# Kernel optimization log

Hardware: AMD Instinct MI355X
Metric: run time of the kernel (lower is better)

The kernel has to match this reference:

```python
import jax, jax.numpy as jnp
import numpy as np

PD = 256            # pretrain_dim == dim_in (standard mode)
DZ = 128            # dim_z
PD2 = PD + 2        # feature dim after concatenating 2-d coords
FD = PD + 2 * PD2   # final_dim = 772
TEMP = float(DZ) ** 0.5
EPS = 1e-12
N1, N2 = 4096, 2048


def _lin_init(key, din, dout):
    w = jax.random.normal(key, (dout, din), jnp.float32) * 0.02
    b = jnp.zeros((dout,), jnp.float32)
    return w, b


def _lin(x, w, b):
    return x @ w.T + b


def setup_inputs() -> dict:
    key = jax.random.key(0)
    ks = jax.random.split(key, 13)
    lm_X = jax.random.normal(ks[0], (N1, PD), jnp.float32)
    lm_Y = jax.random.normal(ks[1], (N1, 2), jnp.float32)
    tg_X = jax.random.normal(ks[2], (N2, PD), jnp.float32)
    tg_Y = jax.random.normal(ks[3], (N2, 2), jnp.float32)
    lm_delay = jax.random.uniform(ks[4], (N1,), jnp.float32)
    tg_delay = jax.random.uniform(ks[5], (N2,), jnp.float32)
    aq_w, aq_b = _lin_init(ks[6], PD, DZ)    # att_attribute q proj
    ak_w, ak_b = _lin_init(ks[7], PD, DZ)    # att_attribute k proj
    w1_w, w1_b = _lin_init(ks[8], PD2, PD2)  # self.w_1
    w2_w, w2_b = _lin_init(ks[9], PD2, PD2)  # self.w_2
    pq_w, pq_b = _lin_init(ks[10], FD, DZ)   # pred attention q proj
    pk_w, pk_b = _lin_init(ks[11], PD, DZ)   # pred attention k proj
    pv_w, pv_b = _lin_init(ks[12], 2, 2)     # pred attention v proj
    gamma1 = jnp.ones((1, 1), jnp.float32)
    gamma2 = jnp.ones((1, 1), jnp.float32)
    gamma3 = jnp.ones((1, 1), jnp.float32)
    alpha = jnp.ones((1, 1), jnp.float32)
    beta = jnp.zeros((1, 1), jnp.float32)
    return dict(lm_X=lm_X, lm_Y=lm_Y, tg_X=tg_X, tg_Y=tg_Y,
                lm_delay=lm_delay, tg_delay=tg_delay,
                aq_w=aq_w, aq_b=aq_b, ak_w=ak_w, ak_b=ak_b,
                w1_w=w1_w, w1_b=w1_b, w2_w=w2_w, w2_b=w2_b,
                pq_w=pq_w, pq_b=pq_b, pk_w=pk_w, pk_b=pk_b,
                pv_w=pv_w, pv_b=pv_b,
                gamma1=gamma1, gamma2=gamma2, gamma3=gamma3,
                alpha=alpha, beta=beta)


def reference(lm_X, lm_Y, tg_X, tg_Y, lm_delay, tg_delay,
              aq_w, aq_b, ak_w, ak_b,
              w1_w, w1_b, w2_w, w2_b,
              pq_w, pq_b, pk_w, pk_b, pv_w, pv_b,
              gamma1, gamma2, gamma3, alpha, beta):
    n2 = tg_X.shape[0]
    a = alpha[0, 0]
    b0 = beta[0, 0]

    lm_feature = jnp.concatenate([lm_X, lm_Y], axis=1)            # [N1, PD2]
    tg_feature_0 = jnp.concatenate([tg_X, jnp.zeros((n2, 2), lm_X.dtype)], axis=1)
    router_0 = jnp.mean(lm_feature, axis=0)                        # [PD2]

    delay_score = jnp.exp(-gamma1[0, 0] * (a * lm_delay + b0))     # [N1]
    rou0 = jnp.exp(-gamma2[0, 0] * (a * tg_delay + b0))            # [N2]
    rou1 = jnp.exp(-gamma3[0, 0] * (a * tg_delay + b0))            # [N2]

    # SimpleAttention1: attribute score of targets over landmarks
    q = _lin(tg_X, aq_w, aq_b)
    k = _lin(lm_X, ak_w, ak_b)
    attr = jnp.exp(jax.nn.softmax((q / TEMP) @ k.T, axis=-1))      # [N2, N1]

    # Degree-normalized propagation of adj_matrix_0 (block-structured:
    # lm rows = identity, tg rows = [attr | I | rou0-col], router row = [delay | 0 | 1]).
    deg_tg0 = 1.0 + attr.sum(axis=1) + rou0                        # [N2]
    tg_prop0 = (attr @ lm_feature + tg_feature_0 + rou0[:, None] * router_0[None, :]) \
               / (deg_tg0 + EPS)[:, None]
    router_prop0 = (delay_score @ lm_feature + router_0) / (1.0 + delay_score.sum() + EPS)

    tg_feature_1 = _lin(tg_prop0, w1_w, w1_b)                      # [N2, PD2]
    router_1 = _lin(router_prop0[None, :], w1_w, w1_b)             # [1, PD2]

    # Second propagation: adj_matrix_1 = I + rou1 on tg->router column.
    tg_prop1 = (tg_feature_1 + rou1[:, None] * router_1) / (1.0 + rou1 + EPS)[:, None]
    tg_feature_2 = _lin(tg_prop1, w2_w, w2_b)                      # [N2, PD2]

    final_tg_feature = jnp.concatenate([tg_X, tg_feature_1, tg_feature_2], axis=-1)  # [N2, FD]

    # SimpleAttention2 (collaborative MLP prediction)
    q2 = _lin(final_tg_feature, pq_w, pq_b)
    k2 = _lin(lm_X, pk_w, pk_b)
    v2 = _lin(lm_Y, pv_w, pv_b)
    attn2 = jax.nn.softmax((q2 / TEMP) @ k2.T, axis=-1)            # [N2, N1]
    y_pred = attn2 @ v2                                            # [N2, 2]
    return y_pred, final_tg_feature
```

## Files before the change

kernel.cpp:

```cpp
#include <hip/hip_runtime.h>

#define N1 4096
#define N2 2048
#define PD 256
#define DZ 128
#define PD2 258
#define PD2P 264
#define FD 772
#define FDP 776
#define APN 272
#define APLD 72
#define SPLITS 16

typedef short s8v __attribute__((ext_vector_type(8)));
typedef float f32x4 __attribute__((ext_vector_type(4)));

__device__ __forceinline__ short f2b(float f) {
    union { float f; unsigned u; } v; v.f = f;
    unsigned r = v.u + 0x7fffu + ((v.u >> 16) & 1u);
    return (short)(r >> 16);
}
__device__ __forceinline__ float sb2f(short s) {
    union { unsigned u; float f; } v;
    v.u = ((unsigned)(unsigned short)s) << 16;
    return v.f;
}

constexpr int R0 = N2 * PD;
constexpr int R1 = R0 + PD2 * PD2P;
constexpr int R2 = R1 + PD2 * PD2P;
constexpr int R3 = R2 + DZ * FDP;
constexpr int R4 = R3 + APN * N1;
constexpr int R5 = R4 + 4096;
constexpr int R6 = R5 + 2048;
constexpr int R7 = R6 + N2 * 4;
constexpr int R8 = R7 + N2 * 6;

__global__ __launch_bounds__(256) void cvt_all(
    const float* __restrict__ lmX, const float* __restrict__ lmY,
    const float* __restrict__ tgX,
    const float* __restrict__ pqw, const float* __restrict__ w1w,
    const float* __restrict__ w2w,
    const float* __restrict__ lmd, const float* __restrict__ tgd,
    const float* __restrict__ g1, const float* __restrict__ g2,
    const float* __restrict__ g3, const float* __restrict__ al,
    const float* __restrict__ be,
    const float* __restrict__ pvw, const float* __restrict__ pvb,
    short* __restrict__ w1wb, short* __restrict__ w2wb,
    short* __restrict__ pqwb, short* __restrict__ lmFTb,
    float* __restrict__ dscore, float* __restrict__ rou0,
    float* __restrict__ rou1, float* __restrict__ v2b,
    float* __restrict__ Z, short* __restrict__ finalFb,
    short* __restrict__ tgp1b, float* __restrict__ outF)
{
    int i = blockIdx.x * 256 + threadIdx.x;
    if (i < R0) { int r = i >> 8, c = i & 255;
                  float v = tgX[i];
                  outF[(size_t)r * FD + c] = v;
                  finalFb[(size_t)r * FDP + c] = f2b(v); return; }
    if (i < R1) { int j = i - R0; int r = j / PD2P, c = j - r * PD2P;
                  w1wb[j] = (c < PD2) ? f2b(w1w[r * PD2 + c]) : (short)0; return; }
    if (i < R2) { int j = i - R1; int r = j / PD2P, c = j - r * PD2P;
                  w2wb[j] = (c < PD2) ? f2b(w2w[r * PD2 + c]) : (short)0; return; }
    if (i < R3) { int j = i - R2; int r = j / FDP, c = j - r * FDP;
                  pqwb[j] = (c < FD) ? f2b(pqw[r * FD + c]) : (short)0; return; }
    if (i < R4) { int j = i - R3; int c = j >> 12, r = j & (N1 - 1);
                  float v = 0.f;
                  if (c < PD) v = lmX[(size_t)r * PD + c];
                  else if (c < PD2) v = lmY[r * 2 + (c - PD)];
                  else if (c == PD2) v = 1.0f;
                  lmFTb[j] = f2b(v); return; }
    if (i < R5) { int j = i - R4;
                  float a = al[0], b = be[0];
                  dscore[j] = __expf(-g1[0] * (a * lmd[j] + b));
                  float y0 = lmY[2 * j], y1 = lmY[2 * j + 1];
                  v2b[2 * j]     = pvw[0] * y0 + pvw[1] * y1 + pvb[0];
                  v2b[2 * j + 1] = pvw[2] * y0 + pvw[3] * y1 + pvb[1];
                  if (j < N2) { float t = a * tgd[j] + b;
                                rou0[j] = __expf(-g2[0] * t);
                                rou1[j] = __expf(-g3[0] * t); }
                  return; }
    if (i < R6) { Z[i - R5] = 0.f; return; }
    if (i < R7) { int j = i - R6; int r = j >> 2;
                  finalFb[(size_t)r * FDP + FD + (j & 3)] = 0; return; }
    if (i < R8) { int j = i - R7; int r = j / 6;
                  tgp1b[(size_t)r * PD2P + PD2 + (j - r * 6)] = 0; return; }
}

__global__ __launch_bounds__(256) void rkq_kernel(
    const float* __restrict__ lmX, const float* __restrict__ tgX,
    const float* __restrict__ aqw, const float* __restrict__ aqb,
    const float* __restrict__ akw, const float* __restrict__ akb,
    const float* __restrict__ pkw, const float* __restrict__ pkb,
    const short* __restrict__ lmFTb, const float* __restrict__ dscore,
    float* __restrict__ router0, float* __restrict__ routerp0,
    short* __restrict__ kk, short* __restrict__ qb)
{
    __shared__ __align__(16) short LDS[5120];
    const int j = blockIdx.x, tid = threadIdx.x;
    const int lane = tid & 63, wv = tid >> 6;
    const int wm = wv >> 1, wn = wv & 1;
    const int lm = lane & 15, lq = lane >> 4;
    const f32x4 zero4 = {0.f, 0.f, 0.f, 0.f};

    if (j < 258) {
        float* r1 = (float*)LDS;
        float* r2 = r1 + 256;
        float* r3 = r2 + 256;
        const short* rowp = lmFTb + (size_t)j * N1;
        float s1 = 0.f, s2 = 0.f, s3 = 0.f;
        for (int i = tid; i < N1; i += 256) {
            float v = sb2f(rowp[i]);
            float d = dscore[i];
            s1 += v; s2 += d * v; s3 += d;
        }
        r1[tid] = s1; r2[tid] = s2; r3[tid] = s3; __syncthreads();
        for (int o = 128; o > 0; o >>= 1) {
            if (tid < o) { r1[tid] += r1[tid + o]; r2[tid] += r2[tid + o]; r3[tid] += r3[tid + o]; }
            __syncthreads();
        }
        if (tid == 0) {
            float r0v = r1[0] / (float)N1;
            router0[j] = r0v;
            routerp0[j] = (r2[0] + r0v) / (1.f + r3[0] + 1e-12f);
        }
        return;
    }
    short* Als = LDS;
    short* Bls = LDS + 64 * 40;
    f32x4 acc[2][2] = {{zero4, zero4}, {zero4, zero4}};
    const int r = tid >> 2, cgp = tid & 3;
    if (j < 514) {
        int jt = j - 258;
        int row0 = (jt >> 2) * 64, col0 = (jt & 3) * 64;
        for (int k0 = 0; k0 < 256; k0 += 32) {
            int gk = k0 + cgp * 8;
            const float* ap = lmX + (size_t)(row0 + r) * PD + gk;
            int c = col0 + r;
            const float* bp = (c < 128) ? akw + (size_t)c * PD + gk
                                        : pkw + (size_t)(c - 128) * PD + gk;
            s8v va, vb;
#pragma unroll
            for (int q = 0; q < 8; ++q) { va[q] = f2b(ap[q]); vb[q] = f2b(bp[q]); }
            *(s8v*)(Als + r * 40 + cgp * 8) = va;
            *(s8v*)(Bls + r * 40 + cgp * 8) = vb;
            __syncthreads();
            s8v af[2], bf[2];
#pragma unroll
            for (int mt = 0; mt < 2; ++mt)
                af[mt] = *(const s8v*)(Als + (wm * 32 + mt * 16 + lm) * 40 + lq * 8);
#pragma unroll
            for (int nt = 0; nt < 2; ++nt)
                bf[nt] = *(const s8v*)(Bls + (wn * 32 + nt * 16 + lm) * 40 + lq * 8);
#pragma unroll
            for (int mt = 0; mt < 2; ++mt)
#pragma unroll
                for (int nt = 0; nt < 2; ++nt)
                    acc[mt][nt] = __builtin_amdgcn_mfma_f32_16x16x32_bf16(
                        af[mt], bf[nt], acc[mt][nt], 0, 0, 0);
            __syncthreads();
        }
#pragma unroll
        for (int mt = 0; mt < 2; ++mt)
#pragma unroll
            for (int nt = 0; nt < 2; ++nt) {
                int c = col0 + wn * 32 + nt * 16 + lm;
                float bv = (c < 128) ? akb[c] : pkb[c - 128];
#pragma unroll
                for (int i = 0; i < 4; ++i) {
                    int rr = row0 + wm * 32 + mt * 16 + lq * 4 + i;
                    kk[(size_t)rr * 256 + c] = f2b(acc[mt][nt][i] + bv);
                }
            }
    } else {
        int jt = j - 514;
        int row0 = (jt >> 1) * 64, col0 = (jt & 1) * 64;
        for (int k0 = 0; k0 < 256; k0 += 32) {
            int gk = k0 + cgp * 8;
            const float* ap = tgX + (size_t)(row0 + r) * PD + gk;
            const float* bp = aqw + (size_t)(col0 + r) * PD + gk;
            s8v va, vb;
#pragma unroll
            for (int q = 0; q < 8; ++q) { va[q] = f2b(ap[q]); vb[q] = f2b(bp[q]); }
            *(s8v*)(Als + r * 40 + cgp * 8) = va;
            *(s8v*)(Bls + r * 40 + cgp * 8) = vb;
            __syncthreads();
            s8v af[2], bf[2];
#pragma unroll
            for (int mt = 0; mt < 2; ++mt)
                af[mt] = *(const s8v*)(Als + (wm * 32 + mt * 16 + lm) * 40 + lq * 8);
#pragma unroll
            for (int nt = 0; nt < 2; ++nt)
                bf[nt] = *(const s8v*)(Bls + (wn * 32 + nt * 16 + lm) * 40 + lq * 8);
#pragma unroll
            for (int mt = 0; mt < 2; ++mt)
#pragma unroll
                for (int nt = 0; nt < 2; ++nt)
                    acc[mt][nt] = __builtin_amdgcn_mfma_f32_16x16x32_bf16(
                        af[mt], bf[nt], acc[mt][nt], 0, 0, 0);
            __syncthreads();
        }
        const float INV_TEMP = 0.08838834764831845f;
#pragma unroll
        for (int mt = 0; mt < 2; ++mt)
#pragma unroll
            for (int nt = 0; nt < 2; ++nt) {
                int c = col0 + wn * 32 + nt * 16 + lm;
                float bv = aqb[c];
#pragma unroll
                for (int i = 0; i < 4; ++i) {
                    int rr = row0 + wm * 32 + mt * 16 + lq * 4 + i;
                    qb[(size_t)rr * DZ + c] = f2b(INV_TEMP * (acc[mt][nt][i] + bv));
                }
            }
    }
}

__global__ __launch_bounds__(256) void scores_e(
    const short* __restrict__ Q, const short* __restrict__ Kk,
    short* __restrict__ E, float* __restrict__ Z,
    const float* __restrict__ rp0, const float* __restrict__ w1w,
    const float* __restrict__ w1b, float* __restrict__ router1)
{
    const int j = blockIdx.x, tid = threadIdx.x;
    if (j == 512) {
        for (int c = tid; c < PD2; c += 256) {
            float s = w1b[c];
            const float* wr = w1w + (size_t)c * PD2;
            for (int k = 0; k < PD2; ++k) s += rp0[k] * wr[k];
            router1[c] = s;
        }
        return;
    }
    __shared__ __align__(16) short LDS[10240];
    short* Als = LDS;
    short* Bls = LDS + 128 * 40;
    const int lane = tid & 63, wv = tid >> 6;
    const int wm = wv >> 1, wn = wv & 1;
    const int lm = lane & 15, lq = lane >> 4;
    const int row0 = (j >> 5) * 128, col0 = (j & 31) * 128;
    const f32x4 zero4 = {0.f, 0.f, 0.f, 0.f};
    f32x4 acc[4][4];
#pragma unroll
    for (int mt = 0; mt < 4; ++mt)
#pragma unroll
        for (int nt = 0; nt < 4; ++nt) acc[mt][nt] = zero4;
    for (int k0 = 0; k0 < 128; k0 += 32) {
#pragma unroll
        for (int l = 0; l < 2; ++l) {
            int id = l * 256 + tid;
            int r = id >> 2, cgp = id & 3;
            int gk = k0 + cgp * 8;
            *(s8v*)(Als + r * 40 + cgp * 8) = *(const s8v*)(Q + (size_t)(row0 + r) * DZ + gk);
            *(s8v*)(Bls + r * 40 + cgp * 8) = *(const s8v*)(Kk + (size_t)(col0 + r) * 256 + gk);
        }
        __syncthreads();
        s8v af[4], bf[4];
#pragma unroll
        for (int mt = 0; mt < 4; ++mt)
            af[mt] = *(const s8v*)(Als + (wm * 64 + mt * 16 + lm) * 40 + lq * 8);
#pragma unroll
        for (int nt = 0; nt < 4; ++nt)
            bf[nt] = *(const s8v*)(Bls + (wn * 64 + nt * 16 + lm) * 40 + lq * 8);
#pragma unroll
        for (int mt = 0; mt < 4; ++mt)
#pragma unroll
            for (int nt = 0; nt < 4; ++nt)
                acc[mt][nt] = __builtin_amdgcn_mfma_f32_16x16x32_bf16(
                    af[mt], bf[nt], acc[mt][nt], 0, 0, 0);
        __syncthreads();
    }
#pragma unroll
    for (int mt = 0; mt < 4; ++mt)
#pragma unroll
        for (int i = 0; i < 4; ++i) {
            int r = row0 + wm * 64 + mt * 16 + lq * 4 + i;
            float rs = 0.f;
#pragma unroll
            for (int nt = 0; nt < 4; ++nt) {
                int c = col0 + wn * 64 + nt * 16 + lm;
                float e = __expf(acc[mt][nt][i]);
                E[(size_t)r * N1 + c] = f2b(e);
                rs += e;
            }
#pragma unroll
            for (int msk = 1; msk < 16; msk <<= 1) rs += __shfl_xor(rs, msk, 64);
            if (lm == 0) atomicAdd(&Z[r], rs);
        }
}

__global__ __launch_bounds__(512) void ap_gemm(const short* __restrict__ E,
                                               const float* __restrict__ Z,
                                               const short* __restrict__ lmFTb,
                                               short* __restrict__ part)
{
    __shared__ __align__(16) short LDS[28800];
    const int tid = threadIdx.x, bid = blockIdx.x;
    const int lane = tid & 63, w8 = tid >> 6;
    const int lm = lane & 15, lq = lane >> 4;
    const int s = bid & 15, row0 = (bid >> 4) * 128;
    const int kbase = s * (N1 / SPLITS);
    short* Als = LDS;
    short* Bls = LDS + 128 * APLD;
    const f32x4 zero4 = {0.f, 0.f, 0.f, 0.f};
    f32x4 acc[17];
#pragma unroll
    for (int nt = 0; nt < 17; ++nt) acc[nt] = zero4;
    for (int it = 0; it < (N1 / SPLITS) / 64; ++it) {
        int k0 = kbase + it * 64;
#pragma unroll
        for (int l = 0; l < 2; ++l) {
            int id = l * 512 + tid;
            int r = id >> 3, gg = id & 7;
            s8v ev = *(const s8v*)(E + (size_t)(row0 + r) * N1 + k0 + gg * 8);
            float invZ = __builtin_amdgcn_rcpf(Z[row0 + r]);
            s8v av;
#pragma unroll
            for (int q = 0; q < 8; ++q)
                av[q] = f2b(__expf(sb2f(ev[q]) * invZ));
            *(s8v*)(Als + r * APLD + gg * 8) = av;
        }
#pragma unroll
        for (int l = 0; l < 5; ++l) {
            int id = l * 512 + tid;
            if (id < APN * 8) {
                int r = id >> 3, gg = id & 7;
                *(s8v*)(Bls + r * APLD + gg * 8) =
                    *(const s8v*)(lmFTb + (size_t)r * N1 + k0 + gg * 8);
            }
        }
        __syncthreads();
        s8v a0 = *(const s8v*)(Als + (w8 * 16 + lm) * APLD + lq * 8);
        s8v a1 = *(const s8v*)(Als + (w8 * 16 + lm) * APLD + 32 + lq * 8);
#pragma unroll
        for (int nt = 0; nt < 17; ++nt) {
            s8v b0 = *(const s8v*)(Bls + (nt * 16 + lm) * APLD + lq * 8);
            s8v b1 = *(const s8v*)(Bls + (nt * 16 + lm) * APLD + 32 + lq * 8);
            acc[nt] = __builtin_amdgcn_mfma_f32_16x16x32_bf16(a0, b0, acc[nt], 0, 0, 0);
            acc[nt] = __builtin_amdgcn_mfma_f32_16x16x32_bf16(a1, b1, acc[nt], 0, 0, 0);
        }
        __syncthreads();
    }
    short* op = part + (size_t)s * N2 * APN;
#pragma unroll
    for (int nt = 0; nt < 17; ++nt) {
        int c = nt * 16 + lm;
#pragma unroll
        for (int i = 0; i < 4; ++i) {
            int r = row0 + w8 * 16 + lq * 4 + i;
            op[(size_t)r * APN + c] = f2b(acc[nt][i]);
        }
    }
}

__global__ __launch_bounds__(256) void fix_tgp0(const short* __restrict__ part,
                                                const float* __restrict__ tgX,
                                                const float* __restrict__ rou0,
                                                const float* __restrict__ router0,
                                                short* __restrict__ outb) {
    int r = blockIdx.x;
    int tid = threadIdx.x;
    __shared__ float sAsum;
    float s0 = 0.f, s1 = 0.f;
#pragma unroll
    for (int s = 0; s < SPLITS; ++s)
        s0 += sb2f(part[((size_t)s * N2 + r) * APN + tid]);
    if (tid < 8) {
#pragma unroll
        for (int s = 0; s < SPLITS; ++s)
            s1 += sb2f(part[((size_t)s * N2 + r) * APN + 256 + tid]);
    }
    if (tid == 2) sAsum = s1;
    __syncthreads();
    float ro = rou0[r];
    float inv = 1.f / (1.f + sAsum + ro + 1e-12f);
    {
        float v = (s0 + tgX[(size_t)r * PD + tid] + ro * router0[tid]) * inv;
        outb[(size_t)r * PD2P + tid] = f2b(v);
    }
    if (tid < 8) {
        int c = 256 + tid;
        float v = 0.f;
        if (c < PD2) v = (s1 + ro * router0[c]) * inv;
        outb[(size_t)r * PD2P + c] = f2b(v);
    }
}

__global__ __launch_bounds__(256) void w_gemm(
    const short* __restrict__ A, const short* __restrict__ B,
    const float* __restrict__ bias,
    float* __restrict__ outFcol, short* __restrict__ fFbcol,
    const float* __restrict__ rou1, const float* __restrict__ router1,
    short* __restrict__ tgp1b)
{
    __shared__ __align__(16) short LDS[5120];
    short* Als = LDS;
    short* Bls = LDS + 64 * 40;
    const int tid = threadIdx.x;
    const int lane = tid & 63, wv = tid >> 6;
    const int wm = wv >> 1, wn = wv & 1;
    const int lm = lane & 15, lq = lane >> 4;
    const int row0 = blockIdx.y * 64, col0 = blockIdx.x * 64;
    const f32x4 zero4 = {0.f, 0.f, 0.f, 0.f};
    f32x4 acc[2][2] = {{zero4, zero4}, {zero4, zero4}};
    const s8v zero8 = {0, 0, 0, 0, 0, 0, 0, 0};
    const int r = tid >> 2, cgp = tid & 3;
    for (int k0 = 0; k0 < PD2P; k0 += 32) {
        int gk = k0 + cgp * 8;
        s8v va = zero8, vb = zero8;
        if (gk < PD2P) {
            va = *(const s8v*)(A + (size_t)(row0 + r) * PD2P + gk);
            if (col0 + r < PD2) vb = *(const s8v*)(B + (size_t)(col0 + r) * PD2P + gk);
        }
        *(s8v*)(Als + r * 40 + cgp * 8) = va;
        *(s8v*)(Bls + r * 40 + cgp * 8) = vb;
        __syncthreads();
        s8v af[2], bf[2];
#pragma unroll
        for (int mt = 0; mt < 2; ++mt)
            af[mt] = *(const s8v*)(Als + (wm * 32 + mt * 16 + lm) * 40 + lq * 8);
#pragma unroll
        for (int nt = 0; nt < 2; ++nt)
            bf[nt] = *(const s8v*)(Bls + (wn * 32 + nt * 16 + lm) * 40 + lq * 8);
#pragma unroll
        for (int mt = 0; mt < 2; ++mt)
#pragma unroll
            for (int nt = 0; nt < 2; ++nt)
                acc[mt][nt] = __builtin_amdgcn_mfma_f32_16x16x32_bf16(
                    af[mt], bf[nt], acc[mt][nt], 0, 0, 0);
        __syncthreads();
    }
#pragma unroll
    for (int mt = 0; mt < 2; ++mt)
#pragma unroll
        for (int nt = 0; nt < 2; ++nt) {
            int c = col0 + wn * 32 + nt * 16 + lm;
            if (c >= PD2) continue;
            float bv = bias[c];
            float rc = router1 ? router1[c] : 0.f;
#pragma unroll
            for (int i = 0; i < 4; ++i) {
                int rr = row0 + wm * 32 + mt * 16 + lq * 4 + i;
                float v = acc[mt][nt][i] + bv;
                outFcol[(size_t)rr * FD + c] = v;
                fFbcol[(size_t)rr * FDP + c] = f2b(v);
                if (tgp1b) {
                    float ro = rou1[rr];
                    tgp1b[(size_t)rr * PD2P + c] =
                        f2b((v + ro * rc) / (1.f + ro + 1e-12f));
                }
            }
        }
}

__global__ __launch_bounds__(256) void q2_gemm(
    const short* __restrict__ A, const short* __restrict__ B,
    const float* __restrict__ bias, short* __restrict__ outB)
{
    __shared__ __align__(16) short LDS[5120];
    short* Als = LDS;
    short* Bls = LDS + 64 * 40;
    const int tid = threadIdx.x;
    const int lane = tid & 63, wv = tid >> 6;
    const int wm = wv >> 1, wn = wv & 1;
    const int lm = lane & 15, lq = lane >> 4;
    const int row0 = blockIdx.y * 64, col0 = blockIdx.x * 64;
    const f32x4 zero4 = {0.f, 0.f, 0.f, 0.f};
    f32x4 acc[2][2] = {{zero4, zero4}, {zero4, zero4}};
    const s8v zero8 = {0, 0, 0, 0, 0, 0, 0, 0};
    const int r = tid >> 2, cgp = tid & 3;
    for (int k0 = 0; k0 < FDP; k0 += 32) {
        int gk = k0 + cgp * 8;
        s8v va = zero8, vb = zero8;
        if (gk < FDP) {
            va = *(const s8v*)(A + (size_t)(row0 + r) * FDP + gk);
            vb = *(const s8v*)(B + (size_t)(col0 + r) * FDP + gk);
        }
        *(s8v*)(Als + r * 40 + cgp * 8) = va;
        *(s8v*)(Bls + r * 40 + cgp * 8) = vb;
        __syncthreads();
        s8v af[2], bf[2];
#pragma unroll
        for (int mt = 0; mt < 2; ++mt)
            af[mt] = *(const s8v*)(Als + (wm * 32 + mt * 16 + lm) * 40 + lq * 8);
#pragma unroll
        for (int nt = 0; nt < 2; ++nt)
            bf[nt] = *(const s8v*)(Bls + (wn * 32 + nt * 16 + lm) * 40 + lq * 8);
#pragma unroll
        for (int mt = 0; mt < 2; ++mt)
#pragma unroll
            for (int nt = 0; nt < 2; ++nt)
                acc[mt][nt] = __builtin_amdgcn_mfma_f32_16x16x32_bf16(
                    af[mt], bf[nt], acc[mt][nt], 0, 0, 0);
        __syncthreads();
    }
    const float INV_TEMP = 0.08838834764831845f;
#pragma unroll
    for (int mt = 0; mt < 2; ++mt)
#pragma unroll
        for (int nt = 0; nt < 2; ++nt) {
            int c = col0 + wn * 32 + nt * 16 + lm;
            float bv = bias[c];
#pragma unroll
            for (int i = 0; i < 4; ++i) {
                int rr = row0 + wm * 32 + mt * 16 + lq * 4 + i;
                outB[(size_t)rr * DZ + c] = f2b(INV_TEMP * (acc[mt][nt][i] + bv));
            }
        }
}

__global__ __launch_bounds__(256) void attn2_flash(
    const short* __restrict__ Q, const short* __restrict__ Kk,
    const float* __restrict__ V, float* __restrict__ part2)
{
    __shared__ __align__(16) short Qls[64 * 136];
    __shared__ __align__(16) short Kls[64 * 136];
    __shared__ float Vls[128];
    const int tid = threadIdx.x;
    const int lane = tid & 63, wv = tid >> 6;
    const int lm = lane & 15, lq = lane >> 4;
    const int chunk = blockIdx.x & 15, row0 = (blockIdx.x >> 4) * 64;
    const f32x4 zero4 = {0.f, 0.f, 0.f, 0.f};
#pragma unroll
    for (int l = 0; l < 4; ++l) {
        int id = l * 256 + tid;
        int r = id >> 4, g = id & 15;
        *(s8v*)(Qls + r * 136 + g * 8) = *(const s8v*)(Q + (size_t)(row0 + r) * DZ + g * 8);
    }
    __syncthreads();
    s8v af[4];
#pragma unroll
    for (int ks = 0; ks < 4; ++ks)
        af[ks] = *(const s8v*)(Qls + (wv * 16 + lm) * 136 + ks * 32 + lq * 8);
    float z[4] = {0.f, 0.f, 0.f, 0.f};
    float y0[4] = {0.f, 0.f, 0.f, 0.f};
    float y1[4] = {0.f, 0.f, 0.f, 0.f};
    for (int t = 0; t < 4; ++t) {
        int col0 = chunk * 256 + t * 64;
        __syncthreads();
#pragma unroll
        for (int l = 0; l < 4; ++l) {
            int id = l * 256 + tid;
            int r = id >> 4, g = id & 15;
            *(s8v*)(Kls + r * 136 + g * 8) =
                *(const s8v*)(Kk + (size_t)(col0 + r) * 256 + 128 + g * 8);
        }
        if (tid < 128) Vls[tid] = V[col0 * 2 + tid];
        __syncthreads();
        f32x4 acc[4];
#pragma unroll
        for (int nt = 0; nt < 4; ++nt) acc[nt] = zero4;
#pragma unroll
        for (int nt = 0; nt < 4; ++nt)
#pragma unroll
            for (int ks = 0; ks < 4; ++ks) {
                s8v bf = *(const s8v*)(Kls + (nt * 16 + lm) * 136 + ks * 32 + lq * 8);
                acc[nt] = __builtin_amdgcn_mfma_f32_16x16x32_bf16(af[ks], bf, acc[nt], 0, 0, 0);
            }
        float v0[4], v1[4];
#pragma unroll
        for (int nt = 0; nt < 4; ++nt) {
            v0[nt] = Vls[(nt * 16 + lm) * 2];
            v1[nt] = Vls[(nt * 16 + lm) * 2 + 1];
        }
#pragma unroll
        for (int i = 0; i < 4; ++i) {
            float e0 = __expf(acc[0][i]), e1 = __expf(acc[1][i]);
            float e2 = __expf(acc[2][i]), e3 = __expf(acc[3][i]);
            z[i]  += e0 + e1 + e2 + e3;
            y0[i] += e0 * v0[0] + e1 * v0[1] + e2 * v0[2] + e3 * v0[3];
            y1[i] += e0 * v1[0] + e1 * v1[1] + e2 * v1[2] + e3 * v1[3];
        }
    }
#pragma unroll
    for (int i = 0; i < 4; ++i) {
#pragma unroll
        for (int msk = 1; msk < 16; msk <<= 1) {
            z[i]  += __shfl_xor(z[i], msk, 64);
            y0[i] += __shfl_xor(y0[i], msk, 64);
            y1[i] += __shfl_xor(y1[i], msk, 64);
        }
    }
    if (lm == 0) {
#pragma unroll
        for (int i = 0; i < 4; ++i) {
            int r = row0 + wv * 16 + lq * 4 + i;
            float* pp = part2 + ((size_t)r * 16 + chunk) * 4;
            pp[0] = z[i]; pp[1] = y0[i]; pp[2] = y1[i];
        }
    }
}

__global__ void attn2_combine(const float* __restrict__ part2, float* __restrict__ out) {
    int r = blockIdx.x * 256 + threadIdx.x;
    if (r >= N2) return;
    const float* pp = part2 + (size_t)r * 64;
    float Zt = 0.f, Y0 = 0.f, Y1 = 0.f;
#pragma unroll
    for (int c = 0; c < 16; ++c) {
        Zt += pp[c * 4]; Y0 += pp[c * 4 + 1]; Y1 += pp[c * 4 + 2];
    }
    out[2 * r] = Y0 / Zt;
    out[2 * r + 1] = Y1 / Zt;
}

extern "C" void kernel_launch(void* const* d_in, const int* in_sizes, int n_in,
                              void* d_out, int out_size, void* d_ws, size_t ws_size,
                              hipStream_t stream) {
    const float* lm_X = (const float*)d_in[0];
    const float* lm_Y = (const float*)d_in[1];
    const float* tg_X = (const float*)d_in[2];
    const float* lm_delay = (const float*)d_in[4];
    const float* tg_delay = (const float*)d_in[5];
    const float* aq_w = (const float*)d_in[6];
    const float* aq_b = (const float*)d_in[7];
    const float* ak_w = (const float*)d_in[8];
    const float* ak_b = (const float*)d_in[9];
    const float* w1_w = (const float*)d_in[10];
    const float* w1_b = (const float*)d_in[11];
    const float* w2_w = (const float*)d_in[12];
    const float* w2_b = (const float*)d_in[13];
    const float* pq_w = (const float*)d_in[14];
    const float* pq_b = (const float*)d_in[15];
    const float* pk_w = (const float*)d_in[16];
    const float* pk_b = (const float*)d_in[17];
    const float* pv_w = (const float*)d_in[18];
    const float* pv_b = (const float*)d_in[19];
    const float* g1 = (const float*)d_in[20];
    const float* g2 = (const float*)d_in[21];
    const float* g3 = (const float*)d_in[22];
    const float* al = (const float*)d_in[23];
    const float* be = (const float*)d_in[24];

    float* out = (float*)d_out;
    float* outF = out + (size_t)N2 * 2;

    char* base = (char*)d_ws;
    size_t off = 0;
    auto allocF = [&](size_t n) -> float* {
        float* q = (float*)(base + off);
        off += (n * 4 + 255) / 256 * 256;
        return q;
    };
    auto allocS = [&](size_t n) -> short* {
        short* q = (short*)(base + off);
        off += (n * 2 + 255) / 256 * 256;
        return q;
    };

    short* E        = allocS((size_t)N2 * N1);
    short* appart   = allocS((size_t)SPLITS * N2 * APN);
    short* lmFTb    = allocS((size_t)APN * N1);
    short* qb       = allocS((size_t)N2 * DZ);
    short* kk       = allocS((size_t)N1 * 256);
    short* q2       = allocS((size_t)N2 * DZ);
    short* tgp0b    = allocS((size_t)N2 * PD2P);
    short* tgp1b    = allocS((size_t)N2 * PD2P);
    short* finalFb  = allocS((size_t)N2 * FDP);
    short* w1wb     = allocS((size_t)PD2 * PD2P);
    short* w2wb     = allocS((size_t)PD2 * PD2P);
    short* pqwb     = allocS((size_t)DZ * FDP);
    float* v2b      = allocF((size_t)N1 * 2);
    float* part2    = allocF((size_t)N2 * 64);
    float* Zbuf     = allocF(N2);
    float* router0  = allocF(PD2);
    float* routerp0 = allocF(PD2);
    float* router1  = allocF(PD2);
    float* dscore   = allocF(N1);
    float* rou0     = allocF(N2);
    float* rou1     = allocF(N2);

    hipLaunchKernelGGL(cvt_all, dim3((R8 + 255) / 256), dim3(256), 0, stream,
                       lm_X, lm_Y, tg_X, pq_w, w1_w, w2_w,
                       lm_delay, tg_delay, g1, g2, g3, al, be, pv_w, pv_b,
                       w1wb, w2wb, pqwb, lmFTb,
                       dscore, rou0, rou1, v2b, Zbuf, finalFb, tgp1b, outF);
    hipLaunchKernelGGL(rkq_kernel, dim3(578), dim3(256), 0, stream,
                       lm_X, tg_X, aq_w, aq_b, ak_w, ak_b, pk_w, pk_b,
                       lmFTb, dscore, router0, routerp0, kk, qb);
    hipLaunchKernelGGL(scores_e, dim3(513), dim3(256), 0, stream,
                       qb, kk, E, Zbuf, routerp0, w1_w, w1_b, router1);
    hipLaunchKernelGGL(ap_gemm, dim3(256), dim3(512), 0, stream, E, Zbuf, lmFTb, appart);
    hipLaunchKernelGGL(fix_tgp0, dim3(N2), dim3(256), 0, stream,
                       appart, tg_X, rou0, router0, tgp0b);
    hipLaunchKernelGGL(w_gemm, dim3(5, 32), dim3(256), 0, stream,
                       tgp0b, w1wb, w1_b, outF + 256, finalFb + 256, rou1, router1, tgp1b);
    hipLaunchKernelGGL(w_gemm, dim3(5, 32), dim3(256), 0, stream,
                       tgp1b, w2wb, w2_b, outF + 514, finalFb + 514,
                       nullptr, nullptr, nullptr);
    hipLaunchKernelGGL(q2_gemm, dim3(2, 32), dim3(256), 0, stream,
                       finalFb, pqwb, pq_b, q2);
    hipLaunchKernelGGL(attn2_flash, dim3(512), dim3(256), 0, stream,
                       q2, kk, v2b, part2);
    hipLaunchKernelGGL(attn2_combine, dim3(8), dim3(256), 0, stream, part2, out);
}
```

Measured before the change: 219.4 us.

## Fold w1/w2 chain into combined weight, pre-convert inputs, fuse combine via atomics

Precomputes the combined weight W2·W1 so tg_feature_1 and tg_feature_2 come from tgp0 in a single merged GEMM launch, with the router and bias terms folded in algebraically. Converts lm_X, tg_X and the projection weights to bf16 once, and computes the router column sums inside the conversion kernel through an LDS transpose. The separate attn2 combine kernel is replaced by atomic accumulation and a last-block-done counter. This removes two launches and a serial GEMM dependency, at the cost of extra precompute, bf16 rounding of the combined weight, and atomic contention.

```diff
diff --git a/kernel.cpp b/kernel.cpp
--- a/kernel.cpp
+++ b/kernel.cpp
@@ -26,53 +26,126 @@
     return v.f;
 }
 
-constexpr int R0 = N2 * PD;
-constexpr int R1 = R0 + PD2 * PD2P;
-constexpr int R2 = R1 + PD2 * PD2P;
-constexpr int R3 = R2 + DZ * FDP;
-constexpr int R4 = R3 + APN * N1;
-constexpr int R5 = R4 + 4096;
-constexpr int R6 = R5 + 2048;
-constexpr int R7 = R6 + N2 * 4;
-constexpr int R8 = R7 + N2 * 6;
+constexpr int Q0 = N2 * PD;
+constexpr int Q1 = Q0 + PD2 * PD2P;
+constexpr int Q2 = Q1 + PD2 * PD2P;
+constexpr int Q3 = Q2 + PD2 * PD2P;
+constexpr int Q4 = Q3 + DZ * FDP;
+constexpr int Q5 = Q4 + 3 * DZ * PD;
+constexpr int Q6 = Q5 + 16 * N1;
+constexpr int Q7 = Q6 + N1;
+constexpr int Q8 = Q7 + N2;
+constexpr int Q9 = Q8 + N2 * 4;
+constexpr int Q10 = Q9 + N2 * 4;
+constexpr int Q11 = Q10 + 256;
+constexpr int TB = 256;
+constexpr int CVT_GRID = TB + (Q11 + 255) / 256;
 
 __global__ __launch_bounds__(256) void cvt_all(
     const float* __restrict__ lmX, const float* __restrict__ lmY,
     const float* __restrict__ tgX,
-    const float* __restrict__ pqw, const float* __restrict__ w1w,
-    const float* __restrict__ w2w,
+    const float* __restrict__ aqw, const float* __restrict__ akw,
+    const float* __restrict__ pkw, const float* __restrict__ pqw,
+    const float* __restrict__ w1w, const float* __restrict__ w2w,
     const float* __restrict__ lmd, const float* __restrict__ tgd,
     const float* __restrict__ g1, const float* __restrict__ g2,
     const float* __restrict__ g3, const float* __restrict__ al,
     const float* __restrict__ be,
     const float* __restrict__ pvw, const float* __restrict__ pvb,
     short* __restrict__ w1wb, short* __restrict__ w2wb,
-    short* __restrict__ pqwb, short* __restrict__ lmFTb,
-    float* __restrict__ dscore, float* __restrict__ rou0,
-    float* __restrict__ rou1, float* __restrict__ v2b,
-    float* __restrict__ Z, short* __restrict__ finalFb,
-    short* __restrict__ tgp1b, float* __restrict__ outF)
+    short* __restrict__ w1wtb, short* __restrict__ pqwb,
+    short* __restrict__ aqwb, short* __restrict__ akwb,
+    short* __restrict__ pkwb, short* __restrict__ lmXb,
+    short* __restrict__ tgXb, short* __restrict__ lmFTb,
+    float* __restrict__ rou0, float* __restrict__ rou1,
+    float* __restrict__ v2b, float* __restrict__ Z,
+    short* __restrict__ finalFb, float* __restrict__ outF,
+    float* __restrict__ r1part, float* __restrict__ r2part,
+    float* __restrict__ p2acc, unsigned* __restrict__ cnt)
 {
-    int i = blockIdx.x * 256 + threadIdx.x;
-    if (i < R0) { int r = i >> 8, c = i & 255;
-                  float v = tgX[i];
+    __shared__ __align__(16) short T[64][72];
+    __shared__ float dsc[64];
+    __shared__ float sp1[4][64];
+    __shared__ float sp2[4][64];
+    const int tid = threadIdx.x;
+
+    if (blockIdx.x < TB) {
+        const int rb = blockIdx.x >> 2, cb = blockIdx.x & 3;
+        const int r0 = rb * 64, c0 = cb * 64;
+        const int rr = tid >> 2, cg = tid & 3;
+        const float* src = lmX + (size_t)(r0 + rr) * PD + c0 + cg * 16;
+        f32x4 f0 = *(const f32x4*)(src);
+        f32x4 f1 = *(const f32x4*)(src + 4);
+        f32x4 f2v = *(const f32x4*)(src + 8);
+        f32x4 f3v = *(const f32x4*)(src + 12);
+        s8v h0, h1;
+#pragma unroll
+        for (int q = 0; q < 4; ++q) {
+            h0[q] = f2b(f0[q]); h0[4 + q] = f2b(f1[q]);
+            h1[q] = f2b(f2v[q]); h1[4 + q] = f2b(f3v[q]);
+        }
+        short* xb = lmXb + (size_t)(r0 + rr) * PD + c0 + cg * 16;
+        *(s8v*)(xb) = h0; *(s8v*)(xb + 8) = h1;
+        *(s8v*)(&T[rr][cg * 16]) = h0;
+        *(s8v*)(&T[rr][cg * 16 + 8]) = h1;
+        if (cg == 0) dsc[rr] = __expf(-g1[0] * (al[0] * lmd[r0 + rr] + be[0]));
+        __syncthreads();
+        {
+            const int c = tid & 63, q = tid >> 6;
+            float s1 = 0.f, s2 = 0.f;
+#pragma unroll
+            for (int k = 0; k < 16; ++k) {
+                float x = sb2f(T[q * 16 + k][c]);
+                s1 += x; s2 += dsc[q * 16 + k] * x;
+            }
+            sp1[q][c] = s1; sp2[q][c] = s2;
+        }
+        __syncthreads();
+        if (tid < 64) {
+            float S1 = sp1[0][tid] + sp1[1][tid] + sp1[2][tid] + sp1[3][tid];
+            float S2 = sp2[0][tid] + sp2[1][tid] + sp2[2][tid] + sp2[3][tid];
+            r1part[(size_t)(c0 + tid) * 64 + rb] = S1;
+            r2part[(size_t)(c0 + tid) * 64 + rb] = S2;
+        }
+        {
+            const int c = tid >> 2, seg = tid & 3;
+            s8v o0, o1;
+#pragma unroll
+            for (int k = 0; k < 8; ++k) {
+                o0[k] = T[seg * 16 + k][c];
+                o1[k] = T[seg * 16 + 8 + k][c];
+            }
+            short* dst = lmFTb + (size_t)(c0 + c) * N1 + r0 + seg * 16;
+            *(s8v*)(dst) = o0; *(s8v*)(dst + 8) = o1;
+        }
+        return;
+    }
+
+    int i = (blockIdx.x - TB) * 256 + tid;
+    if (i < Q0) { int r = i >> 8, c = i & 255;
+                  float v = tgX[i]; short h = f2b(v);
                   outF[(size_t)r * FD + c] = v;
-                  finalFb[(size_t)r * FDP + c] = f2b(v); return; }
-    if (i < R1) { int j = i - R0; int r = j / PD2P, c = j - r * PD2P;
+                  finalFb[(size_t)r * FDP + c] = h;
+                  tgXb[i] = h; return; }
+    if (i < Q1) { int j = i - Q0; int r = j / PD2P, c = j - r * PD2P;
                   w1wb[j] = (c < PD2) ? f2b(w1w[r * PD2 + c]) : (short)0; return; }
-    if (i < R2) { int j = i - R1; int r = j / PD2P, c = j - r * PD2P;
+    if (i < Q2) { int j = i - Q1; int r = j / PD2P, c = j - r * PD2P;
                   w2wb[j] = (c < PD2) ? f2b(w2w[r * PD2 + c]) : (short)0; return; }
-    if (i < R3) { int j = i - R2; int r = j / FDP, c = j - r * FDP;
+    if (i < Q3) { int j = i - Q2; int r = j / PD2P, c = j - r * PD2P;
+                  w1wtb[j] = (c < PD2) ? f2b(w1w[c * PD2 + r]) : (short)0; return; }
+    if (i < Q4) { int j = i - Q3; int r = j / FDP, c = j - r * FDP;
                   pqwb[j] = (c < FD) ? f2b(pqw[r * FD + c]) : (short)0; return; }
-    if (i < R4) { int j = i - R3; int c = j >> 12, r = j & (N1 - 1);
+    if (i < Q5) { int j = i - Q4; int w = j >> 15, idx = j & 32767;
+                  const float* s = (w == 0) ? aqw : (w == 1) ? akw : pkw;
+                  short* d = (w == 0) ? aqwb : (w == 1) ? akwb : pkwb;
+                  d[idx] = f2b(s[idx]); return; }
+    if (i < Q6) { int j = i - Q5; int c = 256 + (j >> 12), r = j & (N1 - 1);
                   float v = 0.f;
-                  if (c < PD) v = lmX[(size_t)r * PD + c];
-                  else if (c < PD2) v = lmY[r * 2 + (c - PD)];
+                  if (c < PD2) v = lmY[2 * r + (c - 256)];
                   else if (c == PD2) v = 1.0f;
-                  lmFTb[j] = f2b(v); return; }
-    if (i < R5) { int j = i - R4;
+                  lmFTb[(size_t)c * N1 + r] = f2b(v); return; }
+    if (i < Q7) { int j = i - Q6;
                   float a = al[0], b = be[0];
-                  dscore[j] = __expf(-g1[0] * (a * lmd[j] + b));
                   float y0 = lmY[2 * j], y1 = lmY[2 * j + 1];
                   v2b[2 * j]     = pvw[0] * y0 + pvw[1] * y1 + pvb[0];
                   v2b[2 * j + 1] = pvw[2] * y0 + pvw[3] * y1 + pvb[1];
@@ -80,68 +153,42 @@
                                 rou0[j] = __expf(-g2[0] * t);
                                 rou1[j] = __expf(-g3[0] * t); }
                   return; }
-    if (i < R6) { Z[i - R5] = 0.f; return; }
-    if (i < R7) { int j = i - R6; int r = j >> 2;
+    if (i < Q8) { Z[i - Q7] = 0.f; return; }
+    if (i < Q9) { int j = i - Q8; int r = j >> 2;
                   finalFb[(size_t)r * FDP + FD + (j & 3)] = 0; return; }
-    if (i < R8) { int j = i - R7; int r = j / 6;
-                  tgp1b[(size_t)r * PD2P + PD2 + (j - r * 6)] = 0; return; }
+    if (i < Q10) { p2acc[i - Q9] = 0.f; return; }
+    if (i < Q11) { int j = i - Q10; if (j < 32) cnt[j] = 0u; return; }
 }
 
 __global__ __launch_bounds__(256) void rkq_kernel(
-    const float* __restrict__ lmX, const float* __restrict__ tgX,
-    const float* __restrict__ aqw, const float* __restrict__ aqb,
-    const float* __restrict__ akw, const float* __restrict__ akb,
-    const float* __restrict__ pkw, const float* __restrict__ pkb,
-    const short* __restrict__ lmFTb, const float* __restrict__ dscore,
-    float* __restrict__ router0, float* __restrict__ routerp0,
-    short* __restrict__ kk, short* __restrict__ qb)
+    const short* __restrict__ lmXb, const short* __restrict__ tgXb,
+    const short* __restrict__ aqwb, const short* __restrict__ akwb,
+    const short* __restrict__ pkwb,
+    const float* __restrict__ aqb, const float* __restrict__ akb,
+    const float* __restrict__ pkb,
+    const short* __restrict__ w2wb, const short* __restrict__ w1wtb,
+    short* __restrict__ kk, short* __restrict__ qb, short* __restrict__ wcb)
 {
     __shared__ __align__(16) short LDS[5120];
+    short* Als = LDS;
+    short* Bls = LDS + 64 * 40;
     const int j = blockIdx.x, tid = threadIdx.x;
     const int lane = tid & 63, wv = tid >> 6;
     const int wm = wv >> 1, wn = wv & 1;
     const int lm = lane & 15, lq = lane >> 4;
     const f32x4 zero4 = {0.f, 0.f, 0.f, 0.f};
-
-    if (j < 258) {
-        float* r1 = (float*)LDS;
-        float* r2 = r1 + 256;
-        float* r3 = r2 + 256;
-        const short* rowp = lmFTb + (size_t)j * N1;
-        float s1 = 0.f, s2 = 0.f, s3 = 0.f;
-        for (int i = tid; i < N1; i += 256) {
-            float v = sb2f(rowp[i]);
-            float d = dscore[i];
-            s1 += v; s2 += d * v; s3 += d;
-        }
-        r1[tid] = s1; r2[tid] = s2; r3[tid] = s3; __syncthreads();
-        for (int o = 128; o > 0; o >>= 1) {
-            if (tid < o) { r1[tid] += r1[tid + o]; r2[tid] += r2[tid + o]; r3[tid] += r3[tid + o]; }
-            __syncthreads();
-        }
-        if (tid == 0) {
-            float r0v = r1[0] / (float)N1;
-            router0[j] = r0v;
-            routerp0[j] = (r2[0] + r0v) / (1.f + r3[0] + 1e-12f);
-        }
-        return;
-    }
-    short* Als = LDS;
-    short* Bls = LDS + 64 * 40;
+    const s8v zero8 = {0, 0, 0, 0, 0, 0, 0, 0};
     f32x4 acc[2][2] = {{zero4, zero4}, {zero4, zero4}};
     const int r = tid >> 2, cgp = tid & 3;
-    if (j < 514) {
-        int jt = j - 258;
-        int row0 = (jt >> 2) * 64, col0 = (jt & 3) * 64;
+
+    if (j < 256) {
+        int row0 = (j >> 2) * 64, col0 = (j & 3) * 64;
         for (int k0 = 0; k0 < 256; k0 += 32) {
             int gk = k0 + cgp * 8;
-            const float* ap = lmX + (size_t)(row0 + r) * PD + gk;
             int c = col0 + r;
-            const float* bp = (c < 128) ? akw + (size_t)c * PD + gk
-                                        : pkw + (size_t)(c - 128) * PD + gk;
-            s8v va, vb;
-#pragma unroll
-            for (int q = 0; q < 8; ++q) { va[q] = f2b(ap[q]); vb[q] = f2b(bp[q]); }
+            s8v va = *(const s8v*)(lmXb + (size_t)(row0 + r) * PD + gk);
+            s8v vb = (c < 128) ? *(const s8v*)(akwb + (size_t)c * PD + gk)
+                               : *(const s8v*)(pkwb + (size_t)(c - 128) * PD + gk);
             *(s8v*)(Als + r * 40 + cgp * 8) = va;
             *(s8v*)(Bls + r * 40 + cgp * 8) = vb;
             __syncthreads();
@@ -172,16 +219,13 @@
                     kk[(size_t)rr * 256 + c] = f2b(acc[mt][nt][i] + bv);
                 }
             }
-    } else {
-        int jt = j - 514;
+    } else if (j < 320) {
+        int jt = j - 256;
         int row0 = (jt >> 1) * 64, col0 = (jt & 1) * 64;
         for (int k0 = 0; k0 < 256; k0 += 32) {
             int gk = k0 + cgp * 8;
-            const float* ap = tgX + (size_t)(row0 + r) * PD + gk;
-            const float* bp = aqw + (size_t)(col0 + r) * PD + gk;
-            s8v va, vb;
-#pragma unroll
-            for (int q = 0; q < 8; ++q) { va[q] = f2b(ap[q]); vb[q] = f2b(bp[q]); }
+            s8v va = *(const s8v*)(tgXb + (size_t)(row0 + r) * PD + gk);
+            s8v vb = *(const s8v*)(aqwb + (size_t)(col0 + r) * PD + gk);
             *(s8v*)(Als + r * 40 + cgp * 8) = va;
             *(s8v*)(Bls + r * 40 + cgp * 8) = vb;
             __syncthreads();
@@ -213,22 +257,120 @@
                     qb[(size_t)rr * DZ + c] = f2b(INV_TEMP * (acc[mt][nt][i] + bv));
                 }
             }
+    } else {
+        int jt = j - 320;
+        int row0 = (jt / 5) * 64, col0 = (jt % 5) * 64;
+        for (int k0 = 0; k0 < PD2P; k0 += 32) {
+            int gk = k0 + cgp * 8;
+            s8v va = zero8, vb = zero8;
+            if (gk < PD2P) {
+                int c2 = row0 + r;
+                if (c2 < PD2) va = *(const s8v*)(w2wb + (size_t)c2 * PD2P + gk);
+                int c1 = col0 + r;
+                if (c1 < PD2) vb = *(const s8v*)(w1wtb + (size_t)c1 * PD2P + gk);
+            }
+            *(s8v*)(Als + r * 40 + cgp * 8) = va;
+            *(s8v*)(Bls + r * 40 + cgp * 8) = vb;
+            __syncthreads();
+            s8v af[2], bf[2];
+#pragma unroll
+            for (int mt = 0; mt < 2; ++mt)
+                af[mt] = *(const s8v*)(Als + (wm * 32 + mt * 16 + lm) * 40 + lq * 8);
+#pragma unroll
+            for (int nt = 0; nt < 2; ++nt)
+                bf[nt] = *(const s8v*)(Bls + (wn * 32 + nt * 16 + lm) * 40 + lq * 8);
+#pragma unroll
+            for (int mt = 0; mt < 2; ++mt)
+#pragma unroll
+                for (int nt = 0; nt < 2; ++nt)
+                    acc[mt][nt] = __builtin_amdgcn_mfma_f32_16x16x32_bf16(
+                        af[mt], bf[nt], acc[mt][nt], 0, 0, 0);
+            __syncthreads();
+        }
+#pragma unroll
+        for (int mt = 0; mt < 2; ++mt)
+#pragma unroll
+            for (int nt = 0; nt < 2; ++nt) {
+                int c = col0 + wn * 32 + nt * 16 + lm;
+                if (c >= PD2P) continue;
+#pragma unroll
+                for (int i = 0; i < 4; ++i) {
+                    int rr = row0 + wm * 32 + mt * 16 + lq * 4 + i;
+                    if (rr < PD2) wcb[(size_t)rr * PD2P + c] = f2b(acc[mt][nt][i]);
+                }
+            }
     }
 }
 
 __global__ __launch_bounds__(256) void scores_e(
-    const short* __restrict__ Q, const short* __restrict__ Kk,
+    const short* __restrict__ Qb, const short* __restrict__ Kk,
     short* __restrict__ E, float* __restrict__ Z,
-    const float* __restrict__ rp0, const float* __restrict__ w1w,
-    const float* __restrict__ w1b, float* __restrict__ router1)
+    const float* __restrict__ r1part, const float* __restrict__ r2part,
+    const float* __restrict__ lmY, const float* __restrict__ lmd,
+    const float* __restrict__ g1, const float* __restrict__ al,
+    const float* __restrict__ be,
+    const float* __restrict__ w1w, const float* __restrict__ w1b,
+    const float* __restrict__ w2w,
+    float* __restrict__ router0, float* __restrict__ rr2,
+    float* __restrict__ u0)
 {
     const int j = blockIdx.x, tid = threadIdx.x;
     if (j == 512) {
+        __shared__ float rp0s[PD2];
+        __shared__ float r1s[PD2];
+        __shared__ float red[256];
+        float S1 = 0.f, S2 = 0.f;
+        {
+            const float* p1 = r1part + (size_t)tid * 64;
+            const float* p2 = r2part + (size_t)tid * 64;
+            for (int k = 0; k < 64; ++k) { S1 += p1[k]; S2 += p2[k]; }
+        }
+        float a_ = al[0], b_ = be[0], gg = g1[0];
+        float sd = 0.f, sdy0 = 0.f, sdy1 = 0.f, sy0 = 0.f, sy1 = 0.f;
+        for (int rr_ = tid; rr_ < N1; rr_ += 256) {
+            float d = __expf(-gg * (a_ * lmd[rr_] + b_));
+            float y0v = lmY[2 * rr_], y1v = lmY[2 * rr_ + 1];
+            sd += d; sdy0 += d * y0v; sdy1 += d * y1v; sy0 += y0v; sy1 += y1v;
+        }
+        float tot[5]; float in5[5] = {sd, sdy0, sdy1, sy0, sy1};
+        for (int t = 0; t < 5; ++t) {
+            __syncthreads();
+            red[tid] = in5[t];
+            __syncthreads();
+            for (int o = 128; o > 0; o >>= 1) {
+                if (tid < o) red[tid] += red[tid + o];
+                __syncthreads();
+            }
+            tot[t] = red[0];
+        }
+        float invd = 1.f / (1.f + tot[0] + 1e-12f);
+        {
+            float r0v = S1 * (1.f / (float)N1);
+            router0[tid] = r0v;
+            rp0s[tid] = (S2 + r0v) * invd;
+        }
+        if (tid == 0) {
+            float r0a = tot[3] * (1.f / (float)N1);
+            float r0b = tot[4] * (1.f / (float)N1);
+            router0[256] = r0a; router0[257] = r0b;
+            rp0s[256] = (tot[1] + r0a) * invd;
+            rp0s[257] = (tot[2] + r0b) * invd;
+        }
+        __syncthreads();
         for (int c = tid; c < PD2; c += 256) {
             float s = w1b[c];
             const float* wr = w1w + (size_t)c * PD2;
-            for (int k = 0; k < PD2; ++k) s += rp0[k] * wr[k];
-            router1[c] = s;
+            for (int k = 0; k < PD2; ++k) s += wr[k] * rp0s[k];
+            r1s[c] = s;
+        }
+        __syncthreads();
+        for (int c = tid; c < PD2; c += 256) {
+            float s2v = 0.f, su = 0.f;
+            const float* wr = w2w + (size_t)c * PD2;
+            for (int k = 0; k < PD2; ++k) {
+                float w = wr[k]; s2v += w * r1s[k]; su += w * w1b[k];
+            }
+            rr2[c] = s2v; u0[c] = su;
         }
         return;
     }
@@ -251,7 +393,7 @@
             int id = l * 256 + tid;
             int r = id >> 2, cgp = id & 3;
             int gk = k0 + cgp * 8;
-            *(s8v*)(Als + r * 40 + cgp * 8) = *(const s8v*)(Q + (size_t)(row0 + r) * DZ + gk);
+            *(s8v*)(Als + r * 40 + cgp * 8) = *(const s8v*)(Qb + (size_t)(row0 + r) * DZ + gk);
             *(s8v*)(Bls + r * 40 + cgp * 8) = *(const s8v*)(Kk + (size_t)(col0 + r) * 256 + gk);
         }
         __syncthreads();
@@ -386,12 +528,13 @@
     }
 }
 
-__global__ __launch_bounds__(256) void w_gemm(
-    const short* __restrict__ A, const short* __restrict__ B,
-    const float* __restrict__ bias,
-    float* __restrict__ outFcol, short* __restrict__ fFbcol,
-    const float* __restrict__ rou1, const float* __restrict__ router1,
-    short* __restrict__ tgp1b)
+__global__ __launch_bounds__(256) void w12_gemm(
+    const short* __restrict__ A, const short* __restrict__ B1,
+    const short* __restrict__ B2,
+    const float* __restrict__ b1, const float* __restrict__ b2,
+    const float* __restrict__ rou1, const float* __restrict__ rr2,
+    const float* __restrict__ u0,
+    float* __restrict__ outF, short* __restrict__ finalFb)
 {
     __shared__ __align__(16) short LDS[5120];
     short* Als = LDS;
@@ -400,7 +543,11 @@
     const int lane = tid & 63, wv = tid >> 6;
     const int wm = wv >> 1, wn = wv & 1;
     const int lm = lane & 15, lq = lane >> 4;
-    const int row0 = blockIdx.y * 64, col0 = blockIdx.x * 64;
+    const int bx = blockIdx.x;
+    const int mode2 = bx >= 5;
+    const int col0 = (mode2 ? bx - 5 : bx) * 64;
+    const short* B = mode2 ? B2 : B1;
+    const int row0 = blockIdx.y * 64;
     const f32x4 zero4 = {0.f, 0.f, 0.f, 0.f};
     f32x4 acc[2][2] = {{zero4, zero4}, {zero4, zero4}};
     const s8v zero8 = {0, 0, 0, 0, 0, 0, 0, 0};
@@ -436,19 +583,22 @@
         for (int nt = 0; nt < 2; ++nt) {
             int c = col0 + wn * 32 + nt * 16 + lm;
             if (c >= PD2) continue;
-            float bv = bias[c];
-            float rc = router1 ? router1[c] : 0.f;
 #pragma unroll
             for (int i = 0; i < 4; ++i) {
                 int rr = row0 + wm * 32 + mt * 16 + lq * 4 + i;
-                float v = acc[mt][nt][i] + bv;
-                outFcol[(size_t)rr * FD + c] = v;
-                fFbcol[(size_t)rr * FDP + c] = f2b(v);
-                if (tgp1b) {
+                float v;
+                int co;
+                if (!mode2) {
+                    v = acc[mt][nt][i] + b1[c];
+                    co = 256 + c;
+                } else {
                     float ro = rou1[rr];
-                    tgp1b[(size_t)rr * PD2P + c] =
-                        f2b((v + ro * rc) / (1.f + ro + 1e-12f));
+                    float invd = 1.f / (1.f + ro + 1e-12f);
+                    v = (acc[mt][nt][i] + u0[c] + ro * rr2[c]) * invd + b2[c];
+                    co = 514 + c;
                 }
+                outF[(size_t)rr * FD + co] = v;
+                finalFb[(size_t)rr * FDP + co] = f2b(v);
             }
         }
 }
@@ -511,11 +661,13 @@
 
 __global__ __launch_bounds__(256) void attn2_flash(
     const short* __restrict__ Q, const short* __restrict__ Kk,
-    const float* __restrict__ V, float* __restrict__ part2)
+    const float* __restrict__ V, float* __restrict__ acc4,
+    unsigned* __restrict__ cnt, float* __restrict__ out)
 {
     __shared__ __align__(16) short Qls[64 * 136];
     __shared__ __align__(16) short Kls[64 * 136];
     __shared__ float Vls[128];
+    __shared__ unsigned oldv_s;
     const int tid = threadIdx.x;
     const int lane = tid & 63, wv = tid >> 6;
     const int lm = lane & 15, lq = lane >> 4;
@@ -585,23 +737,25 @@
 #pragma unroll
         for (int i = 0; i < 4; ++i) {
             int r = row0 + wv * 16 + lq * 4 + i;
-            float* pp = part2 + ((size_t)r * 16 + chunk) * 4;
-            pp[0] = z[i]; pp[1] = y0[i]; pp[2] = y1[i];
-        }
-    }
-}
-
-__global__ void attn2_combine(const float* __restrict__ part2, float* __restrict__ out) {
-    int r = blockIdx.x * 256 + threadIdx.x;
-    if (r >= N2) return;
-    const float* pp = part2 + (size_t)r * 64;
-    float Zt = 0.f, Y0 = 0.f, Y1 = 0.f;
-#pragma unroll
-    for (int c = 0; c < 16; ++c) {
-        Zt += pp[c * 4]; Y0 += pp[c * 4 + 1]; Y1 += pp[c * 4 + 2];
-    }
-    out[2 * r] = Y0 / Zt;
-    out[2 * r + 1] = Y1 / Zt;
+            float* pp = acc4 + (size_t)r * 4;
+            atomicAdd(pp + 0, z[i]);
+            atomicAdd(pp + 1, y0[i]);
+            atomicAdd(pp + 2, y1[i]);
+        }
+    }
+    __threadfence();
+    __syncthreads();
+    if (tid == 0) oldv_s = atomicAdd(&cnt[blockIdx.x >> 4], 1u);
+    __syncthreads();
+    if (oldv_s == 15u && tid < 64) {
+        int r = row0 + tid;
+        float* pp = acc4 + (size_t)r * 4;
+        float zt  = atomicAdd(pp + 0, 0.f);
+        float yy0 = atomicAdd(pp + 1, 0.f);
+        float yy1 = atomicAdd(pp + 2, 0.f);
+        out[2 * r] = yy0 / zt;
+        out[2 * r + 1] = yy1 / zt;
+    }
 }
 
 extern "C" void kernel_launch(void* const* d_in, const int* in_sizes, int n_in,
@@ -651,46 +805,53 @@
     short* E        = allocS((size_t)N2 * N1);
     short* appart   = allocS((size_t)SPLITS * N2 * APN);
     short* lmFTb    = allocS((size_t)APN * N1);
-    short* qb       = allocS((size_t)N2 * DZ);
+    short* lmXb     = allocS((size_t)N1 * PD);
+    short* tgXb     = allocS((size_t)N2 * PD);
+    short* qbuf     = allocS((size_t)N2 * DZ);
     short* kk       = allocS((size_t)N1 * 256);
     short* q2       = allocS((size_t)N2 * DZ);
     short* tgp0b    = allocS((size_t)N2 * PD2P);
-    short* tgp1b    = allocS((size_t)N2 * PD2P);
     short* finalFb  = allocS((size_t)N2 * FDP);
     short* w1wb     = allocS((size_t)PD2 * PD2P);
     short* w2wb     = allocS((size_t)PD2 * PD2P);
+    short* w1wtb    = allocS((size_t)PD2 * PD2P);
+    short* wcb      = allocS((size_t)PD2 * PD2P);
     short* pqwb     = allocS((size_t)DZ * FDP);
+    short* aqwb     = allocS((size_t)DZ * PD);
+    short* akwb     = allocS((size_t)DZ * PD);
+    short* pkwb     = allocS((size_t)DZ * PD);
     float* v2b      = allocF((size_t)N1 * 2);
-    float* part2    = allocF((size_t)N2 * 64);
+    float* p2acc    = allocF((size_t)N2 * 4);
     float* Zbuf     = allocF(N2);
     float* router0  = allocF(PD2);
-    float* routerp0 = allocF(PD2);
-    float* router1  = allocF(PD2);
-    float* dscore   = allocF(N1);
+    float* rr2v     = allocF(PD2);
+    float* u0v      = allocF(PD2);
+    float* r1part   = allocF(256 * 64);
+    float* r2part   = allocF(256 * 64);
+    unsigned* cnt   = (unsigned*)allocF(32);
     float* rou0     = allocF(N2);
     float* rou1     = allocF(N2);
 
-    hipLaunchKernelGGL(cvt_all, dim3((R8 + 255) / 256), dim3(256), 0, stream,
-                       lm_X, lm_Y, tg_X, pq_w, w1_w, w2_w,
+    hipLaunchKernelGGL(cvt_all, dim3(CVT_GRID), dim3(256), 0, stream,
+                       lm_X, lm_Y, tg_X, aq_w, ak_w, pk_w, pq_w, w1_w, w2_w,
                        lm_delay, tg_delay, g1, g2, g3, al, be, pv_w, pv_b,
-                       w1wb, w2wb, pqwb, lmFTb,
-                       dscore, rou0, rou1, v2b, Zbuf, finalFb, tgp1b, outF);
-    hipLaunchKernelGGL(rkq_kernel, dim3(578), dim3(256), 0, stream,
-                       lm_X, tg_X, aq_w, aq_b, ak_w, ak_b, pk_w, pk_b,
-                       lmFTb, dscore, router0, routerp0, kk, qb);
+                       w1wb, w2wb, w1wtb, pqwb, aqwb, akwb, pkwb,
+                       lmXb, tgXb, lmFTb, rou0, rou1, v2b, Zbuf,
+                       finalFb, outF, r1part, r2part, p2acc, cnt);
+    hipLaunchKernelGGL(rkq_kernel, dim3(345), dim3(256), 0, stream,
+                       lmXb, tgXb, aqwb, akwb, pkwb, aq_b, ak_b, pk_b,
+                       w2wb, w1wtb, kk, qbuf, wcb);
     hipLaunchKernelGGL(scores_e, dim3(513), dim3(256), 0, stream,
-                       qb, kk, E, Zbuf, routerp0, w1_w, w1_b, router1);
+                       qbuf, kk, E, Zbuf, r1part, r2part, lm_Y, lm_delay,
+                       g1, al, be, w1_w, w1_b, w2_w, router0, rr2v, u0v);
     hipLaunchKernelGGL(ap_gemm, dim3(256), dim3(512), 0, stream, E, Zbuf, lmFTb, appart);
     hipLaunchKernelGGL(fix_tgp0, dim3(N2), dim3(256), 0, stream,
                        appart, tg_X, rou0, router0, tgp0b);
-    hipLaunchKernelGGL(w_gemm, dim3(5, 32), dim3(256), 0, stream,
-                       tgp0b, w1wb, w1_b, outF + 256, finalFb + 256, rou1, router1, tgp1b);
-    hipLaunchKernelGGL(w_gemm, dim3(5, 32), dim3(256), 0, stream,
-                       tgp1b, w2wb, w2_b, outF + 514, finalFb + 514,
-                       nullptr, nullptr, nullptr);
+    hipLaunchKernelGGL(w12_gemm, dim3(10, 32), dim3(256), 0, stream,
+                       tgp0b, w1wb, wcb, w1_b, w2_b, rou1, rr2v, u0v,
+                       outF, finalFb);
     hipLaunchKernelGGL(q2_gemm, dim3(2, 32), dim3(256), 0, stream,
                        finalFb, pqwb, pq_b, q2);
     hipLaunchKernelGGL(attn2_flash, dim3(512), dim3(256), 0, stream,
-                       q2, kk, v2b, part2);
-    hipLaunchKernelGGL(attn2_combine, dim3(8), dim3(256), 0, stream, part2, out);
-}
+                       q2, kk, v2b, p2acc, cnt, out);
+}
```

After: 265.6 us. 21.1% more time.
